# Performance work log

Hardware: AMD Instinct MI355X
Metric: run time of the kernel (lower is better)

The kernel has to match this reference:

```python
import jax, jax.numpy as jnp
import numpy as np
from jax import lax

T = 8192
D_MODEL = 768
D_RNN = 1024
KW = 4  # conv kernel width


def setup_inputs() -> dict:
    key = jax.random.key(0)
    ks = jax.random.split(key, 9)
    x = jax.random.normal(ks[0], (T, D_MODEL), jnp.float32)
    # equinox nn.Linear(in, out): weight [out, in], bias [out]
    w1 = jax.random.normal(ks[1], (2 * D_RNN, D_MODEL), jnp.float32) / np.sqrt(D_MODEL)
    b1 = jnp.zeros((2 * D_RNN,), jnp.float32)
    # nn.Conv1d(d_rnn, d_rnn, 4, use_bias=False): kernel [out_ch, in_ch, kw]
    conv_w = jax.random.normal(ks[2], (D_RNN, D_RNN, KW), jnp.float32) / np.sqrt(D_RNN * KW)
    w_rg = jax.random.normal(ks[3], (2 * D_RNN, D_RNN), jnp.float32) / np.sqrt(D_RNN)
    b_rg = jnp.zeros((2 * D_RNN,), jnp.float32)
    w_out = jax.random.normal(ks[4], (D_MODEL, D_RNN), jnp.float32) / np.sqrt(D_RNN)
    b_out = jnp.zeros((D_MODEL,), jnp.float32)
    # Lambda ~ U(inv_sigmoid(0.9)^{1/8}, inv_sigmoid(0.999)^{1/8}) as in __init__
    inv_sig = lambda p: np.log(1.0 / (1.0 - p))
    lower = np.power(inv_sig(0.9), 1.0 / 8.0)
    upper = np.power(inv_sig(0.999), 1.0 / 8.0)
    Lambda = jax.random.uniform(ks[5], (D_RNN,), jnp.float32, lower, upper)
    return {"x": x, "w1": w1, "b1": b1, "conv_w": conv_w, "w_rg": w_rg,
            "b_rg": b_rg, "w_out": w_out, "b_out": b_out, "Lambda": Lambda}


def _rglru_forward(x, w1, b1, conv_w, w_rg, b_rg, w_out, b_out, Lambda):
    # lin1 then split into gate branch (gelu) and recurrent branch
    h = x @ w1.T + b1                       # [T, 2*D_RNN]
    a_branch = jax.nn.gelu(h[:, :D_RNN])    # [T, D_RNN]
    b_branch = h[:, D_RNN:]                 # [T, D_RNN]
    # causal conv1d: lhs [N=1, C, T], rhs [O, I, KW], left pad 3
    bc = lax.conv_general_dilated(b_branch.T[None], conv_w, (1,), [(KW - 1, 0)])[0].T  # [T, D_RNN]
    # RG-LRU gating
    g = jax.nn.sigmoid(bc @ w_rg.T + b_rg)  # [T, 2*D_RNN]
    inp_gate = g[:, :D_RNN]
    rec_gate = g[:, D_RNN:]
    a_t = jnp.exp(-8.0 * jax.nn.softplus(Lambda)[None, :] * rec_gate)  # [T, D_RNN]
    gated_x = jnp.sqrt(1.0 - a_t ** 2) * inp_gate * bc

    def rec_step(state, xs):
        gx, av = xs
        hn = av * state + gx
        return hn, hn

    _, y = lax.scan(rec_step, jnp.zeros((D_RNN,), x.dtype), (gated_x, a_t))
    return (a_branch * y) @ w_out.T + b_out  # [T, D_MODEL]


def reference(x, w1, b1, conv_w, w_rg, b_rg, w_out, b_out, Lambda):
    return _rglru_forward(x, w1, b1, conv_w, w_rg, b_rg, w_out, b_out, Lambda)
```

## Files before the change

kernel.cpp:

```cpp
#include <hip/hip_runtime.h>
#include <hip/hip_bf16.h>
#include <stdint.h>


#define T_LEN 8192
#define DM 768
#define DR 1024
#define NC 128
#define CL 64

typedef __bf16 bf16x8 __attribute__((ext_vector_type(8)));
typedef float  f32x4  __attribute__((ext_vector_type(4)));

#define AS1 __attribute__((address_space(1)))
#define AS3 __attribute__((address_space(3)))

__device__ __forceinline__ void cp16_g2l(const void* g, void* l) {
    __builtin_amdgcn_global_load_lds((const AS1 void*)g, (AS3 void*)l, 16, 0, 0);
}

__device__ __forceinline__ float gelu_tanh(float x) {
    const float inner = 0.7978845608028654f * (x + 0.044715f * x * x * x);
    return 0.5f * x * (1.f + tanhf(inner));
}

__device__ __forceinline__ __bf16 f2b(float v) {
    __hip_bfloat16 h = __float2bfloat16(v);
    return *reinterpret_cast<__bf16*>(&h);
}

template<int BN, int EPI, bool SHIFT>
__global__ __launch_bounds__(256, 4)
void gemm_mfma(const __hip_bfloat16* __restrict__ A,
               const __hip_bfloat16* __restrict__ B,
               const float* __restrict__ bias,
               void* __restrict__ Cv,
               int K, int lda, int N,
               __hip_bfloat16* __restrict__ D2)
{
    constexpr int NI  = BN / 32;
    constexpr int BLD = (BN * 4) / 256;
    constexpr int NLD = 2 + BLD;
    __shared__ __align__(16) unsigned char smem[32768];
    __bf16* Asb = (__bf16*)smem;
    __bf16* Bsb = (__bf16*)(smem + 16384);

    const int tid  = threadIdx.x;
    const int lane = tid & 63;
    const int wave = tid >> 6;
    const size_t m0 = (size_t)blockIdx.x * 128;
    const int    n0 = blockIdx.y * BN;
    const int wm = (wave >> 1) * 64;
    const int wn = (wave & 1) * (BN / 2);

    f32x4 acc[4][NI];
#pragma unroll
    for (int i = 0; i < 4; ++i)
#pragma unroll
        for (int j = 0; j < NI; ++j)
            acc[i][j] = f32x4{0.f, 0.f, 0.f, 0.f};

    const int frow = lane & 15;
    const int fq   = lane >> 4;

    auto stage = [&](int buf, int k0) {
#pragma unroll
        for (int q = 0; q < 2; ++q) {
            const int lin = q * 256 + tid;
            const int rr  = lin >> 2;
            const int gc  = (lin & 3) ^ ((rr >> 1) & 3);
            const size_t ar = m0 + rr + (SHIFT ? (size_t)(k0 >> 10) : 0);
            const int    ac = SHIFT ? (k0 & 1023) : k0;
            cp16_g2l(A + ar * (size_t)lda + ac + gc * 8, Asb + buf * 4096 + lin * 8);
        }
#pragma unroll
        for (int q = 0; q < BLD; ++q) {
            const int lin = q * 256 + tid;
            const int rr  = lin >> 2;
            const int gc  = (lin & 3) ^ ((rr >> 1) & 3);
            cp16_g2l(B + (size_t)(n0 + rr) * K + k0 + gc * 8,
                     Bsb + buf * (BN * 32) + lin * 8);
        }
    };

    const int nt = K / 32;
    stage(0, 0);
    int cur = 0;
    for (int t = 0; t < nt; ++t) {
        if (t + 1 < nt) {
            stage(cur ^ 1, (t + 1) * 32);
            asm volatile("s_waitcnt vmcnt(%0)" :: "n"(NLD) : "memory");
        } else {
            asm volatile("s_waitcnt vmcnt(0)" ::: "memory");
        }
        __builtin_amdgcn_sched_barrier(0);
        __builtin_amdgcn_s_barrier();
        __builtin_amdgcn_sched_barrier(0);

        bf16x8 af[4], bfr[NI];
#pragma unroll
        for (int mi = 0; mi < 4; ++mi) {
            const int R = wm + mi * 16 + frow;
            af[mi] = *(const bf16x8*)&Asb[cur * 4096 + R * 32 + ((fq ^ ((R >> 1) & 3)) * 8)];
        }
#pragma unroll
        for (int ni = 0; ni < NI; ++ni) {
            const int R = wn + ni * 16 + frow;
            bfr[ni] = *(const bf16x8*)&Bsb[cur * (BN * 32) + R * 32 + ((fq ^ ((R >> 1) & 3)) * 8)];
        }
        asm volatile("s_waitcnt lgkmcnt(0)" ::: "memory");
        __builtin_amdgcn_sched_barrier(0);
        __builtin_amdgcn_s_barrier();
        __builtin_amdgcn_sched_barrier(0);

        __builtin_amdgcn_s_setprio(1);
#pragma unroll
        for (int mi = 0; mi < 4; ++mi)
#pragma unroll
            for (int ni = 0; ni < NI; ++ni)
                acc[mi][ni] = __builtin_amdgcn_mfma_f32_16x16x32_bf16(
                    af[mi], bfr[ni], acc[mi][ni], 0, 0, 0);
        __builtin_amdgcn_s_setprio(0);
        cur ^= 1;
    }

    __syncthreads();
    const int er = fq * 4;
    const int ec = frow;

    if (EPI == 0) {
        float* Cl = (float*)smem;
#pragma unroll
        for (int ni = 0; ni < NI; ++ni) {
            const int cc = wn + ni * 16 + ec;
            const float bv = bias ? bias[n0 + cc] : 0.f;
#pragma unroll
            for (int mi = 0; mi < 4; ++mi)
#pragma unroll
                for (int r2 = 0; r2 < 4; ++r2) {
                    const int R = wm + mi * 16 + er + r2;
                    Cl[R * 64 + ((((cc >> 2) ^ (R & 7)) << 2) | (cc & 3))] =
                        acc[mi][ni][r2] + bv;
                }
        }
        __syncthreads();
        float* outp = (float*)Cv;
#pragma unroll
        for (int p = 0; p < 8; ++p) {
            const int R   = (tid >> 4) + p * 16;
            const int chn = tid & 15;
            const f32x4 v = *(const f32x4*)&Cl[R * 64 + ((chn ^ (R & 7)) << 2)];
            *(f32x4*)&outp[(m0 + R) * (size_t)N + n0 + chn * 4] = v;
        }
    } else {
        __bf16* Cl = (__bf16*)smem;
        const bool ahalf = (EPI == 2) && (n0 < 1024);
#pragma unroll
        for (int ni = 0; ni < NI; ++ni) {
            const int cc = wn + ni * 16 + ec;
            const float bv = bias ? bias[n0 + cc] : 0.f;
#pragma unroll
            for (int mi = 0; mi < 4; ++mi)
#pragma unroll
                for (int r2 = 0; r2 < 4; ++r2) {
                    const int R = wm + mi * 16 + er + r2;
                    float v = acc[mi][ni][r2] + bv;
                    if (EPI == 2 && ahalf) v = gelu_tanh(v);
                    Cl[R * 128 + ((((cc >> 3) ^ (R & 7)) << 3) | (cc & 7))] = f2b(v);
                }
        }
        __syncthreads();
#pragma unroll
        for (int p = 0; p < 8; ++p) {
            const int R   = (tid >> 4) + p * 16;
            const int chn = tid & 15;
            const bf16x8 v = *(const bf16x8*)&Cl[R * 128 + ((chn ^ (R & 7)) << 3)];
            if (EPI == 1) {
                *(bf16x8*)((__bf16*)Cv + (m0 + R) * (size_t)N + n0 + chn * 8) = v;
            } else if (n0 < 1024) {
                *(bf16x8*)((__bf16*)Cv + (m0 + R) * 1024 + n0 + chn * 8) = v;
            } else {
                *(bf16x8*)((__bf16*)D2 + (m0 + R + 3) * 1024 + (n0 - 1024) + chn * 8) = v;
            }
        }
    }
}

#define PREP_X   6291456
#define PREP_W1  (PREP_X + 1572864)
#define PREP_WRG (PREP_W1 + 2097152)
#define PREP_WO  (PREP_WRG + 786432)
#define PREP_CW  (PREP_WO + 4194304)
#define PREP_TOT (PREP_CW + 3072)
__global__ void prep_kernel(const float* __restrict__ x, const float* __restrict__ w1,
                            const float* __restrict__ w_rg, const float* __restrict__ w_out,
                            const float* __restrict__ conv_w,
                            __hip_bfloat16* __restrict__ xb, __hip_bfloat16* __restrict__ w1b,
                            __hip_bfloat16* __restrict__ w_rgb, __hip_bfloat16* __restrict__ w_outb,
                            __hip_bfloat16* __restrict__ wbigb, __hip_bfloat16* __restrict__ bbp)
{
    const int idx = blockIdx.x * 256 + threadIdx.x;
    if (idx < PREP_X) {
        xb[idx] = __float2bfloat16(x[idx]);
    } else if (idx < PREP_W1) {
        const int i = idx - PREP_X;  w1b[i] = __float2bfloat16(w1[i]);
    } else if (idx < PREP_WRG) {
        const int i = idx - PREP_W1; w_rgb[i] = __float2bfloat16(w_rg[i]);
    } else if (idx < PREP_WO) {
        const int i = idx - PREP_WRG; w_outb[i] = __float2bfloat16(w_out[i]);
    } else if (idx < PREP_CW) {
        const int n = idx - PREP_WO;
        const int o = n >> 12, r = n & 4095, k = r >> 10, i = r & 1023;
        wbigb[n] = __float2bfloat16(conv_w[o * 4096 + i * 4 + k]);
    } else {
        bbp[idx - PREP_CW] = __float2bfloat16(0.f);
    }
}

__global__ void scan_pass1(const __hip_bfloat16* __restrict__ gp,
                           const __hip_bfloat16* __restrict__ bc,
                           const float* __restrict__ Lambda,
                           float* __restrict__ ch, float* __restrict__ ca)
{
    const int c = blockIdx.y * 256 + threadIdx.x;
    const int j = blockIdx.x;
    const float cl = -8.f * log1pf(expf(Lambda[c]));
    float h = 0.f, ap = 1.f;
    const int t0 = j * CL;
    for (int tt = 0; tt < CL; ++tt) {
        const int t = t0 + tt;
        const long gi = (long)t * 2048 + c;
        const float ig = 1.f / (1.f + expf(-__bfloat162float(gp[gi])));
        const float rg = 1.f / (1.f + expf(-__bfloat162float(gp[gi + 1024])));
        const float a  = expf(cl * rg);
        const float gx = sqrtf(fmaxf(0.f, 1.f - a * a)) * ig *
                         __bfloat162float(bc[(long)t * 1024 + c]);
        h  = fmaf(a, h, gx);
        ap *= a;
    }
    ch[j * 1024 + c] = h;
    ca[j * 1024 + c] = ap;
}

__global__ void scan_combine(float* __restrict__ ch, const float* __restrict__ ca)
{
    const int c = blockIdx.x * 256 + threadIdx.x;
    float carry = 0.f;
    for (int j = 0; j < NC; ++j) {
        const float hj = ch[j * 1024 + c];
        const float aj = ca[j * 1024 + c];
        ch[j * 1024 + c] = carry;
        carry = fmaf(aj, carry, hj);
    }
}

__global__ void scan_pass2(const __hip_bfloat16* __restrict__ gp, const __hip_bfloat16* bc,
                           const float* __restrict__ Lambda,
                           const float* __restrict__ carry_in,
                           const __hip_bfloat16* __restrict__ ab,
                           __hip_bfloat16* zb)
{
    const int c = blockIdx.y * 256 + threadIdx.x;
    const int j = blockIdx.x;
    const float cl = -8.f * log1pf(expf(Lambda[c]));
    float h = carry_in[j * 1024 + c];
    const int t0 = j * CL;
    for (int tt = 0; tt < CL; ++tt) {
        const int t = t0 + tt;
        const long gi = (long)t * 2048 + c;
        const long bi = (long)t * 1024 + c;
        const float ig = 1.f / (1.f + expf(-__bfloat162float(gp[gi])));
        const float rg = 1.f / (1.f + expf(-__bfloat162float(gp[gi + 1024])));
        const float a  = expf(cl * rg);
        const float gx = sqrtf(fmaxf(0.f, 1.f - a * a)) * ig * __bfloat162float(bc[bi]);
        h = fmaf(a, h, gx);
        zb[bi] = __float2bfloat16(__bfloat162float(ab[bi]) * h);
    }
}

extern "C" void kernel_launch(void* const* d_in, const int* in_sizes, int n_in,
                              void* d_out, int out_size, void* d_ws, size_t ws_size,
                              hipStream_t stream)
{
    const float* x      = (const float*)d_in[0];
    const float* w1     = (const float*)d_in[1];
    const float* b1     = (const float*)d_in[2];
    const float* conv_w = (const float*)d_in[3];
    const float* w_rg   = (const float*)d_in[4];
    const float* b_rg   = (const float*)d_in[5];
    const float* w_out  = (const float*)d_in[6];
    const float* b_out  = (const float*)d_in[7];
    const float* Lambda = (const float*)d_in[8];
    float* out = (float*)d_out;
    (void)in_sizes; (void)n_in; (void)out_size; (void)ws_size;

    char* p = (char*)d_ws;
    auto alloc = [&](size_t bytes) { char* r = p; p += (bytes + 255) & ~255ULL; return r; };
    __hip_bfloat16* gpre  = (__hip_bfloat16*)alloc(8192ULL * 2048 * 2);
    __hip_bfloat16* ab    = (__hip_bfloat16*)alloc(8192ULL * 1024 * 2);
    __hip_bfloat16* bbp   = (__hip_bfloat16*)alloc(8200ULL * 1024 * 2);
    __hip_bfloat16* bcb   = (__hip_bfloat16*)alloc(8192ULL * 1024 * 2);
    __hip_bfloat16* wbigb = (__hip_bfloat16*)alloc(1024ULL * 4096 * 2);
    __hip_bfloat16* xb    = (__hip_bfloat16*)alloc(8192ULL * 768 * 2);
    __hip_bfloat16* w1b   = (__hip_bfloat16*)alloc(2048ULL * 768 * 2);
    __hip_bfloat16* w_rgb = (__hip_bfloat16*)alloc(2048ULL * 1024 * 2);
    __hip_bfloat16* w_outb= (__hip_bfloat16*)alloc(768ULL * 1024 * 2);
    float*          chv   = (float*)alloc(NC * 1024ULL * 4);
    float*          cav   = (float*)alloc(NC * 1024ULL * 4);
    __hip_bfloat16* zb    = bcb;

    prep_kernel<<<PREP_TOT / 256, 256, 0, stream>>>(x, w1, w_rg, w_out, conv_w,
                                                    xb, w1b, w_rgb, w_outb, wbigb, bbp);

    {
        dim3 grid(T_LEN / 128, 2048 / 128);
        gemm_mfma<128, 2, false><<<grid, 256, 0, stream>>>(xb, w1b, b1, ab, DM, DM, 2048, bbp);
    }

    {
        dim3 grid(T_LEN / 128, 1024 / 128);
        gemm_mfma<128, 1, true><<<grid, 256, 0, stream>>>(bbp, wbigb, nullptr, bcb, 4096, 1024, 1024, nullptr);
    }

    {
        dim3 grid(T_LEN / 128, 2048 / 128);
        gemm_mfma<128, 1, false><<<grid, 256, 0, stream>>>(bcb, w_rgb, b_rg, gpre, DR, DR, 2048, nullptr);
    }

    {
        dim3 gs(NC, DR / 256);
        scan_pass1<<<gs, 256, 0, stream>>>(gpre, bcb, Lambda, chv, cav);
        scan_combine<<<DR / 256, 256, 0, stream>>>(chv, cav);
        scan_pass2<<<gs, 256, 0, stream>>>(gpre, bcb, Lambda, chv, ab, zb);
    }

    {
        dim3 grid(T_LEN / 128, DM / 64);
        gemm_mfma<64, 0, false><<<grid, 256, 0, stream>>>(zb, w_outb, b_out, out, DR, DR, DM, nullptr);
    }
}
```

Measured before the change: 284.0 us.

## Add dedicated conv MFMA kernel reusing A tile across four kernel taps

```diff
diff --git a/kernel.cpp b/kernel.cpp
--- a/kernel.cpp
+++ b/kernel.cpp
@@ -183,6 +183,136 @@
                 *(bf16x8*)((__bf16*)D2 + (m0 + R + 3) * 1024 + (n0 - 1024) + chn * 8) = v;
             }
         }
+    }
+}
+
+__global__ __launch_bounds__(256, 4)
+void conv_mfma(const __hip_bfloat16* __restrict__ bbp,
+               const __hip_bfloat16* __restrict__ W,
+               __hip_bfloat16* __restrict__ C)
+{
+    __shared__ __align__(16) unsigned char smem[33280];
+    __bf16* Ah = (__bf16*)smem;
+    __bf16* Bt = (__bf16*)(smem + 16896);
+
+    const int tid  = threadIdx.x;
+    const int lane = tid & 63;
+    const int wave = tid >> 6;
+    const size_t m0 = (size_t)blockIdx.x * 128;
+    const int    n0 = blockIdx.y * 128;
+    const int wm = (wave >> 1) * 64;
+    const int wn = (wave & 1) * 64;
+
+    f32x4 acc[4][4];
+#pragma unroll
+    for (int i = 0; i < 4; ++i)
+#pragma unroll
+        for (int j = 0; j < 4; ++j)
+            acc[i][j] = f32x4{0.f, 0.f, 0.f, 0.f};
+
+    const int frow = lane & 15;
+    const int fq   = lane >> 4;
+
+    auto stageA = [&](int abuf, int kc) {
+#pragma unroll
+        for (int q = 0; q < 2; ++q) {
+            const int lin = q * 256 + tid;
+            const int rr  = lin >> 2;
+            const int gc  = (lin & 3) ^ ((rr >> 1) & 3);
+            cp16_g2l(bbp + (m0 + rr) * 1024 + kc + gc * 8, Ah + abuf * 4224 + lin * 8);
+        }
+        if (tid < 16) {
+            const int lin = 512 + tid;
+            const int rr  = lin >> 2;
+            const int gc  = (lin & 3) ^ ((rr >> 1) & 3);
+            cp16_g2l(bbp + (m0 + rr) * 1024 + kc + gc * 8, Ah + abuf * 4224 + lin * 8);
+        }
+    };
+    auto stageB = [&](int bbuf, int u) {
+        const int s  = u & 3;
+        const int kc = (u >> 2) * 32;
+#pragma unroll
+        for (int q = 0; q < 2; ++q) {
+            const int lin = q * 256 + tid;
+            const int rr  = lin >> 2;
+            const int gc  = (lin & 3) ^ ((rr >> 1) & 3);
+            cp16_g2l(W + (size_t)(n0 + rr) * 4096 + s * 1024 + kc + gc * 8,
+                     Bt + bbuf * 4096 + lin * 8);
+        }
+    };
+
+    stageA(0, 0);
+    stageB(0, 0);
+    int acur = 0, bcur = 0;
+    for (int u = 0; u < 128; ++u) {
+        const int s = u & 3;
+        if (u + 1 < 128) {
+            stageB(bcur ^ 1, u + 1);
+            if (s == 3) {
+                stageA(acur ^ 1, ((u >> 2) + 1) * 32);
+                asm volatile("s_waitcnt vmcnt(4)" ::: "memory");
+            } else {
+                asm volatile("s_waitcnt vmcnt(2)" ::: "memory");
+            }
+        } else {
+            asm volatile("s_waitcnt vmcnt(0)" ::: "memory");
+        }
+        __builtin_amdgcn_sched_barrier(0);
+        __builtin_amdgcn_s_barrier();
+        __builtin_amdgcn_sched_barrier(0);
+
+        bf16x8 af[4], bfr[4];
+#pragma unroll
+        for (int mi = 0; mi < 4; ++mi) {
+            const int R = wm + mi * 16 + frow + s;
+            af[mi] = *(const bf16x8*)&Ah[acur * 4224 + R * 32 + ((fq ^ ((R >> 1) & 3)) * 8)];
+        }
+#pragma unroll
+        for (int ni = 0; ni < 4; ++ni) {
+            const int R = wn + ni * 16 + frow;
+            bfr[ni] = *(const bf16x8*)&Bt[bcur * 4096 + R * 32 + ((fq ^ ((R >> 1) & 3)) * 8)];
+        }
+        asm volatile("s_waitcnt lgkmcnt(0)" ::: "memory");
+        __builtin_amdgcn_sched_barrier(0);
+        __builtin_amdgcn_s_barrier();
+        __builtin_amdgcn_sched_barrier(0);
+
+        __builtin_amdgcn_s_setprio(1);
+#pragma unroll
+        for (int mi = 0; mi < 4; ++mi)
+#pragma unroll
+            for (int ni = 0; ni < 4; ++ni)
+                acc[mi][ni] = __builtin_amdgcn_mfma_f32_16x16x32_bf16(
+                    af[mi], bfr[ni], acc[mi][ni], 0, 0, 0);
+        __builtin_amdgcn_s_setprio(0);
+
+        bcur ^= 1;
+        if (s == 3) acur ^= 1;
+    }
+
+    __syncthreads();
+    const int er = fq * 4;
+    const int ec = frow;
+    __bf16* Cl = (__bf16*)smem;
+#pragma unroll
+    for (int ni = 0; ni < 4; ++ni) {
+        const int cc = wn + ni * 16 + ec;
+#pragma unroll
+        for (int mi = 0; mi < 4; ++mi)
+#pragma unroll
+            for (int r2 = 0; r2 < 4; ++r2) {
+                const int R = wm + mi * 16 + er + r2;
+                Cl[R * 128 + ((((cc >> 3) ^ (R & 7)) << 3) | (cc & 7))] =
+                    f2b(acc[mi][ni][r2]);
+            }
+    }
+    __syncthreads();
+#pragma unroll
+    for (int p = 0; p < 8; ++p) {
+        const int R   = (tid >> 4) + p * 16;
+        const int chn = tid & 15;
+        const bf16x8 v = *(const bf16x8*)&Cl[R * 128 + ((chn ^ (R & 7)) << 3)];
+        *(bf16x8*)((__bf16*)C + (m0 + R) * 1024 + n0 + chn * 8) = v;
     }
 }
 
@@ -319,7 +449,7 @@
 
     {
         dim3 grid(T_LEN / 128, 1024 / 128);
-        gemm_mfma<128, 1, true><<<grid, 256, 0, stream>>>(bbp, wbigb, nullptr, bcb, 4096, 1024, 1024, nullptr);
+        conv_mfma<<<grid, 256, 0, stream>>>(bbp, wbigb, bcb);
     }
 
     {
```

New measurement: 273.3 us. 1.04x faster.
